# Kernel optimization log

Hardware: AMD Instinct MI355X
Metric: run time of the kernel (lower is better)

## Reference

```python
import jax, jax.numpy as jnp
import numpy as np

C = 64   # in_planes
F = 40   # n_freq
T = 512  # n_frame
B = 16


def setup_inputs() -> dict:
    key = jax.random.key(0)
    kx, kq, kk, kv = jax.random.split(key, 4)
    x = jax.random.normal(kx, (B, C, F, T), dtype=jnp.float32)
    # 1x1 conv weights, no bias: [out_ch, in_ch]
    s = 1.0 / np.sqrt(C)
    Wq = jax.random.uniform(kq, (C, C), dtype=jnp.float32, minval=-s, maxval=s)
    Wk = jax.random.uniform(kk, (C, C), dtype=jnp.float32, minval=-s, maxval=s)
    Wv = jax.random.uniform(kv, (C, C), dtype=jnp.float32, minval=-s, maxval=s)
    return {"x": x, "Wq": Wq, "Wk": Wk, "Wv": Wv}


def _proj_tokens(W, x):
    # 1x1 conv (channel mix) then permute(0,3,2,1) + view -> [B, T, F*C]
    y = jnp.einsum('oc,bcft->btfo', W, x)      # [B, T, F, C]
    b, t, f, c = y.shape
    return y.reshape(b, t, f * c)


def reference(x, Wq, Wk, Wv):
    n_batch, n_planes, n_freq, n_frame = x.shape
    d = n_freq * n_planes
    q = _proj_tokens(Wq, x)                     # [B, T, d]
    k = _proj_tokens(Wk, x)
    v = _proj_tokens(Wv, x)
    scores = jnp.einsum('bqd,bkd->bqk', q, k) / jnp.sqrt(jnp.float32(d))
    attn = jax.nn.softmax(scores, axis=-1)      # [B, T, T]
    out = jnp.einsum('bqk,bkd->bqd', attn, v)   # [B, T, d]
    out = out.reshape(n_batch, n_frame, n_freq, n_planes)
    return jnp.transpose(out, (0, 3, 2, 1))     # [B, C, F, T]
```

## Files before the change

kernel.cpp:

```cpp
#include <hip/hip_runtime.h>

constexpr int B_ = 16, C_ = 64, F_ = 40, T_ = 512;
constexpr int D_ = F_ * C_;
constexpr float SCALE = 0.019764235376052372f;

typedef __attribute__((ext_vector_type(8))) short s16x8;
typedef __attribute__((ext_vector_type(4))) short s16x4;
typedef __attribute__((ext_vector_type(2))) short s16x2;
typedef __attribute__((ext_vector_type(4))) float f32x4;

static __device__ __forceinline__ short f2bf(float f) {
  union { float f; unsigned u; } v; v.f = f;
  unsigned r = v.u + 0x7fffu + ((v.u >> 16) & 1u);
  return (short)(r >> 16);
}

static __device__ __forceinline__ f32x4 mfma16(s16x8 a, s16x8 b, f32x4 c) {
  return __builtin_amdgcn_mfma_f32_16x16x32_bf16(a, b, c, 0, 0, 0);
}

__global__ __launch_bounds__(256) void proj_kernel(
    const float* __restrict__ x,
    const float* __restrict__ Wq, const float* __restrict__ Wk,
    const float* __restrict__ Wv,
    short* __restrict__ Q, short* __restrict__ K, short* __restrict__ V)
{
  constexpr int WS = 72;
  constexpr int XS = 260;
  __shared__ short Wl[3][64 * WS];
  __shared__ short Xl[64 * XS];

  const int b = blockIdx.z, f = blockIdx.y, tt = blockIdx.x;
  const int tid = threadIdx.x;

  for (int i = tid; i < 64 * 64; i += 256) {
    const int o = i >> 6, c = i & 63;
    Wl[0][o * WS + c] = f2bf(Wq[i]);
    Wl[1][o * WS + c] = f2bf(Wk[i]);
    Wl[2][o * WS + c] = f2bf(Wv[i]);
  }
  const float* xp = x + (((size_t)b * 64) * 40 + f) * 512 + tt * 256;
  for (int i = tid; i < 64 * 64; i += 256) {
    const int c = i >> 6, j = i & 63;
    const float4 v4 = *(const float4*)(xp + (size_t)c * (F_ * T_) + j * 4);
    s16x4 s4; s4[0] = f2bf(v4.x); s4[1] = f2bf(v4.y);
    s4[2] = f2bf(v4.z); s4[3] = f2bf(v4.w);
    *(s16x4*)&Xl[c * XS + j * 4] = s4;
  }
  __syncthreads();

  const int w = tid >> 6, lane = tid & 63;
  const int quad = lane >> 4, c16 = lane & 15;
  const int tl = w * 64;

  s16x8 bfrag[4][2];
  #pragma unroll
  for (int ni = 0; ni < 4; ++ni)
    #pragma unroll
    for (int ks = 0; ks < 2; ++ks) {
      const int t = tl + ni * 16 + c16;
      const int cb = ks * 32 + quad * 8;
      s16x8 tmp;
      #pragma unroll
      for (int j = 0; j < 8; ++j) tmp[j] = Xl[(cb + j) * XS + t];
      bfrag[ni][ks] = tmp;
    }

  for (int p = 0; p < 3; ++p) {
    f32x4 acc[4][4] = {};
    #pragma unroll
    for (int ks = 0; ks < 2; ++ks) {
      s16x8 afrag[4];
      #pragma unroll
      for (int mi = 0; mi < 4; ++mi)
        afrag[mi] = *(const s16x8*)&Wl[p][(mi * 16 + c16) * WS + ks * 32 + quad * 8];
      #pragma unroll
      for (int mi = 0; mi < 4; ++mi)
        #pragma unroll
        for (int ni = 0; ni < 4; ++ni)
          acc[mi][ni] = mfma16(afrag[mi], bfrag[ni][ks], acc[mi][ni]);
    }
    if (p < 2) {
      short* outp = (p == 0) ? Q : K;
      #pragma unroll
      for (int mi = 0; mi < 4; ++mi)
        #pragma unroll
        for (int ni = 0; ni < 4; ++ni) {
          const int t = tt * 256 + tl + ni * 16 + c16;
          const int o = mi * 16 + quad * 4;
          s16x4 s4;
          #pragma unroll
          for (int r = 0; r < 4; ++r) s4[r] = f2bf(acc[mi][ni][r]);
          *(s16x4*)&outp[((size_t)(b * 512 + t)) * D_ + f * 64 + o] = s4;
        }
    } else {
      #pragma unroll
      for (int mi = 0; mi < 4; ++mi)
        #pragma unroll
        for (int ni = 0; ni < 4; ++ni) {
          const int t = tt * 256 + tl + ni * 16 + c16;
          #pragma unroll
          for (int r = 0; r < 4; ++r) {
            const int o = mi * 16 + quad * 4 + r;
            V[((size_t)(b * D_ + f * 64 + o)) * 512 + t] = f2bf(acc[mi][ni][r]);
          }
        }
    }
  }
}

__global__ __launch_bounds__(256) void scores_kernel(
    const short* __restrict__ Q, const short* __restrict__ K,
    float* __restrict__ S)
{
  __shared__ short As[128 * 32];
  __shared__ short Bs[128 * 32];
  const int b = blockIdx.y;
  const int mt = blockIdx.x >> 2, nt = blockIdx.x & 3;
  const int m0 = mt * 128, n0 = nt * 128;
  const int tid = threadIdx.x;
  const int w = tid >> 6, lane = tid & 63, quad = lane >> 4, c16 = lane & 15;
  const int wm = (w >> 1) * 64, wn = (w & 1) * 64;
  const int r0 = tid >> 2, cc8 = (tid & 3) * 8;

  const short* qb = Q + (size_t)b * 512 * D_;
  const short* kb = K + (size_t)b * 512 * D_;
  const short* qrow0 = qb + (size_t)(m0 + r0) * D_ + cc8;
  const short* qrow1 = qb + (size_t)(m0 + 64 + r0) * D_ + cc8;
  const short* krow0 = kb + (size_t)(n0 + r0) * D_ + cc8;
  const short* krow1 = kb + (size_t)(n0 + 64 + r0) * D_ + cc8;

  f32x4 acc[4][4] = {};
  s16x8 a0 = *(const s16x8*)(qrow0);
  s16x8 a1 = *(const s16x8*)(qrow1);
  s16x8 b0 = *(const s16x8*)(krow0);
  s16x8 b1 = *(const s16x8*)(krow1);

  constexpr int NK = D_ / 32;
  for (int kk = 0; kk < NK; ++kk) {
    __syncthreads();
    *(s16x8*)&As[r0 * 32 + cc8] = a0;
    *(s16x8*)&As[(64 + r0) * 32 + cc8] = a1;
    *(s16x8*)&Bs[r0 * 32 + cc8] = b0;
    *(s16x8*)&Bs[(64 + r0) * 32 + cc8] = b1;
    __syncthreads();
    if (kk + 1 < NK) {
      const int off = (kk + 1) * 32;
      a0 = *(const s16x8*)(qrow0 + off);
      a1 = *(const s16x8*)(qrow1 + off);
      b0 = *(const s16x8*)(krow0 + off);
      b1 = *(const s16x8*)(krow1 + off);
    }
    s16x8 am[4], bm[4];
    #pragma unroll
    for (int mi = 0; mi < 4; ++mi)
      am[mi] = *(const s16x8*)&As[(wm + mi * 16 + c16) * 32 + quad * 8];
    #pragma unroll
    for (int ni = 0; ni < 4; ++ni)
      bm[ni] = *(const s16x8*)&Bs[(wn + ni * 16 + c16) * 32 + quad * 8];
    #pragma unroll
    for (int mi = 0; mi < 4; ++mi)
      #pragma unroll
      for (int ni = 0; ni < 4; ++ni)
        acc[mi][ni] = mfma16(am[mi], bm[ni], acc[mi][ni]);
  }

  float* sp = S + (size_t)b * 512 * 512;
  #pragma unroll
  for (int mi = 0; mi < 4; ++mi)
    #pragma unroll
    for (int ni = 0; ni < 4; ++ni) {
      const int kcol = n0 + wn + ni * 16 + c16;
      const int qrow = m0 + wm + mi * 16 + quad * 4;
      #pragma unroll
      for (int r = 0; r < 4; ++r)
        sp[(size_t)(qrow + r) * 512 + kcol] = acc[mi][ni][r] * SCALE;
    }
}

__global__ __launch_bounds__(256) void softmax_kernel(
    const float* __restrict__ S, short* __restrict__ A)
{
  const int b = blockIdx.y, q = blockIdx.x;
  const int tid = threadIdx.x, w = tid >> 6, lane = tid & 63;
  const float* row = S + ((size_t)b * 512 + q) * 512;
  float2 v = *(const float2*)(row + tid * 2);

  float m = fmaxf(v.x, v.y);
  #pragma unroll
  for (int off = 1; off < 64; off <<= 1) m = fmaxf(m, __shfl_xor(m, off));
  __shared__ float redm[4], reds[4];
  if (lane == 0) redm[w] = m;
  __syncthreads();
  m = fmaxf(fmaxf(redm[0], redm[1]), fmaxf(redm[2], redm[3]));

  const float e0 = __expf(v.x - m), e1 = __expf(v.y - m);
  float s = e0 + e1;
  #pragma unroll
  for (int off = 1; off < 64; off <<= 1) s += __shfl_xor(s, off);
  if (lane == 0) reds[w] = s;
  __syncthreads();
  s = (reds[0] + reds[1]) + (reds[2] + reds[3]);

  const float inv = 1.0f / s;
  s16x2 o2; o2[0] = f2bf(e0 * inv); o2[1] = f2bf(e1 * inv);
  *(s16x2*)&A[((size_t)b * 512 + q) * 512 + tid * 2] = o2;
}

__global__ __launch_bounds__(256) void pv_kernel(
    const short* __restrict__ A, const short* __restrict__ V,
    float* __restrict__ out)
{
  __shared__ short As[128 * 32];
  __shared__ short Bs[128 * 32];
  const int b = blockIdx.y;
  const int mt = blockIdx.x / 20, dt = blockIdx.x % 20;
  const int m0 = mt * 128, n0 = dt * 128;
  const int tid = threadIdx.x;
  const int w = tid >> 6, lane = tid & 63, quad = lane >> 4, c16 = lane & 15;
  const int wm = (w >> 1) * 64, wn = (w & 1) * 64;
  const int r0 = tid >> 2, cc8 = (tid & 3) * 8;

  const short* ab = A + (size_t)b * 512 * 512;
  const short* vb = V + (size_t)b * D_ * 512;
  const short* arow0 = ab + (size_t)(m0 + r0) * 512 + cc8;
  const short* arow1 = ab + (size_t)(m0 + 64 + r0) * 512 + cc8;
  const short* vrow0 = vb + (size_t)(n0 + r0) * 512 + cc8;
  const short* vrow1 = vb + (size_t)(n0 + 64 + r0) * 512 + cc8;

  f32x4 acc[4][4] = {};
  s16x8 a0 = *(const s16x8*)(arow0);
  s16x8 a1 = *(const s16x8*)(arow1);
  s16x8 b0 = *(const s16x8*)(vrow0);
  s16x8 b1 = *(const s16x8*)(vrow1);

  constexpr int NK = 512 / 32;
  for (int kk = 0; kk < NK; ++kk) {
    __syncthreads();
    *(s16x8*)&As[r0 * 32 + cc8] = a0;
    *(s16x8*)&As[(64 + r0) * 32 + cc8] = a1;
    *(s16x8*)&Bs[r0 * 32 + cc8] = b0;
    *(s16x8*)&Bs[(64 + r0) * 32 + cc8] = b1;
    __syncthreads();
    if (kk + 1 < NK) {
      const int off = (kk + 1) * 32;
      a0 = *(const s16x8*)(arow0 + off);
      a1 = *(const s16x8*)(arow1 + off);
      b0 = *(const s16x8*)(vrow0 + off);
      b1 = *(const s16x8*)(vrow1 + off);
    }
    s16x8 am[4], bm[4];
    #pragma unroll
    for (int mi = 0; mi < 4; ++mi)
      am[mi] = *(const s16x8*)&As[(wm + mi * 16 + c16) * 32 + quad * 8];
    #pragma unroll
    for (int ni = 0; ni < 4; ++ni)
      bm[ni] = *(const s16x8*)&Bs[(wn + ni * 16 + c16) * 32 + quad * 8];
    #pragma unroll
    for (int mi = 0; mi < 4; ++mi)
      #pragma unroll
      for (int ni = 0; ni < 4; ++ni)
        acc[mi][ni] = mfma16(am[mi], bm[ni], acc[mi][ni]);
  }

  #pragma unroll
  for (int mi = 0; mi < 4; ++mi)
    #pragma unroll
    for (int ni = 0; ni < 4; ++ni) {
      const int d = n0 + wn + ni * 16 + c16;
      const int ff = d >> 6, cc = d & 63;
      const int t = m0 + wm + mi * 16 + quad * 4;
      float4 o4;
      o4.x = acc[mi][ni][0]; o4.y = acc[mi][ni][1];
      o4.z = acc[mi][ni][2]; o4.w = acc[mi][ni][3];
      *(float4*)&out[(((size_t)b * 64 + cc) * 40 + ff) * 512 + t] = o4;
    }
}

extern "C" void kernel_launch(void* const* d_in, const int* in_sizes, int n_in,
                              void* d_out, int out_size, void* d_ws, size_t ws_size,
                              hipStream_t stream)
{
  const float* x  = (const float*)d_in[0];
  const float* Wq = (const float*)d_in[1];
  const float* Wk = (const float*)d_in[2];
  const float* Wv = (const float*)d_in[3];
  float* out = (float*)d_out;

  char* ws = (char*)d_ws;
  constexpr size_t QB = (size_t)B_ * T_ * D_ * 2;
  short* Q  = (short*)(ws);
  short* Kt = (short*)(ws + QB);
  short* Vt = (short*)(ws + 2 * QB);
  float* S  = (float*)(ws + 3 * QB);
  short* At = (short*)(ws + 3 * QB + (size_t)B_ * T_ * T_ * 4);

  proj_kernel<<<dim3(2, 40, 16), 256, 0, stream>>>(x, Wq, Wk, Wv, Q, Kt, Vt);
  scores_kernel<<<dim3(16, 16), 256, 0, stream>>>(Q, Kt, S);
  softmax_kernel<<<dim3(512, 16), 256, 0, stream>>>(S, At);
  pv_kernel<<<dim3(80, 16), 256, 0, stream>>>(At, Vt, out);
}
```

Baseline: 305.0 us.

## Rebalance proj/scores grids, vectorize V stores, use per-wave softmax rows

The projection kernel now handles 128 frames per block instead of 256, doubling the grid. It drops the shared-memory weight staging and loads weights into registers straight from global memory. The V projection swaps the MFMA operand order so V can be stored as 4-wide vectors instead of scalar strided stores. The scores kernel halves its M tile to 64, doubling its grid of 256 blocks for better CU occupancy. Softmax now assigns one row per wave with shuffle-only reductions and no block barriers, at the cost of redundant weight conversion per block.

Result: slower. 320.0 us (+4.9%).

```diff
diff --git a/kernel.cpp b/kernel.cpp
--- a/kernel.cpp
+++ b/kernel.cpp
@@ -6,7 +6,6 @@
 
 typedef __attribute__((ext_vector_type(8))) short s16x8;
 typedef __attribute__((ext_vector_type(4))) short s16x4;
-typedef __attribute__((ext_vector_type(2))) short s16x2;
 typedef __attribute__((ext_vector_type(4))) float f32x4;
 
 static __device__ __forceinline__ short f2bf(float f) {
@@ -25,23 +24,17 @@
     const float* __restrict__ Wv,
     short* __restrict__ Q, short* __restrict__ K, short* __restrict__ V)
 {
-  constexpr int WS = 72;
-  constexpr int XS = 260;
-  __shared__ short Wl[3][64 * WS];
+  constexpr int XS = 132;
   __shared__ short Xl[64 * XS];
 
   const int b = blockIdx.z, f = blockIdx.y, tt = blockIdx.x;
   const int tid = threadIdx.x;
 
-  for (int i = tid; i < 64 * 64; i += 256) {
-    const int o = i >> 6, c = i & 63;
-    Wl[0][o * WS + c] = f2bf(Wq[i]);
-    Wl[1][o * WS + c] = f2bf(Wk[i]);
-    Wl[2][o * WS + c] = f2bf(Wv[i]);
-  }
-  const float* xp = x + (((size_t)b * 64) * 40 + f) * 512 + tt * 256;
-  for (int i = tid; i < 64 * 64; i += 256) {
-    const int c = i >> 6, j = i & 63;
+  const float* xp = x + (((size_t)b * 64) * 40 + f) * 512 + tt * 128;
+  #pragma unroll
+  for (int it = 0; it < 8; ++it) {
+    const int i = tid + it * 256;
+    const int c = i >> 5, j = i & 31;
     const float4 v4 = *(const float4*)(xp + (size_t)c * (F_ * T_) + j * 4);
     s16x4 s4; s4[0] = f2bf(v4.x); s4[1] = f2bf(v4.y);
     s4[2] = f2bf(v4.z); s4[3] = f2bf(v4.w);
@@ -51,11 +44,11 @@
 
   const int w = tid >> 6, lane = tid & 63;
   const int quad = lane >> 4, c16 = lane & 15;
-  const int tl = w * 64;
-
-  s16x8 bfrag[4][2];
-  #pragma unroll
-  for (int ni = 0; ni < 4; ++ni)
+  const int tl = w * 32;
+
+  s16x8 bfrag[2][2];
+  #pragma unroll
+  for (int ni = 0; ni < 2; ++ni)
     #pragma unroll
     for (int ks = 0; ks < 2; ++ks) {
       const int t = tl + ni * 16 + c16;
@@ -66,27 +59,38 @@
       bfrag[ni][ks] = tmp;
     }
 
+  #pragma unroll
   for (int p = 0; p < 3; ++p) {
-    f32x4 acc[4][4] = {};
-    #pragma unroll
-    for (int ks = 0; ks < 2; ++ks) {
-      s16x8 afrag[4];
-      #pragma unroll
-      for (int mi = 0; mi < 4; ++mi)
-        afrag[mi] = *(const s16x8*)&Wl[p][(mi * 16 + c16) * WS + ks * 32 + quad * 8];
+    const float* Wp = (p == 0) ? Wq : (p == 1) ? Wk : Wv;
+    s16x8 wfrag[4][2];
+    #pragma unroll
+    for (int mi = 0; mi < 4; ++mi)
+      #pragma unroll
+      for (int ks = 0; ks < 2; ++ks) {
+        const float* wp = Wp + (mi * 16 + c16) * 64 + ks * 32 + quad * 8;
+        const float4 w0 = *(const float4*)(wp);
+        const float4 w1 = *(const float4*)(wp + 4);
+        s16x8 wf;
+        wf[0] = f2bf(w0.x); wf[1] = f2bf(w0.y); wf[2] = f2bf(w0.z); wf[3] = f2bf(w0.w);
+        wf[4] = f2bf(w1.x); wf[5] = f2bf(w1.y); wf[6] = f2bf(w1.z); wf[7] = f2bf(w1.w);
+        wfrag[mi][ks] = wf;
+      }
+
+    if (p < 2) {
+      f32x4 acc[4][2] = {};
+      #pragma unroll
+      for (int ks = 0; ks < 2; ++ks)
+        #pragma unroll
+        for (int mi = 0; mi < 4; ++mi)
+          #pragma unroll
+          for (int ni = 0; ni < 2; ++ni)
+            acc[mi][ni] = mfma16(wfrag[mi][ks], bfrag[ni][ks], acc[mi][ni]);
+      short* outp = (p == 0) ? Q : K;
       #pragma unroll
       for (int mi = 0; mi < 4; ++mi)
         #pragma unroll
-        for (int ni = 0; ni < 4; ++ni)
-          acc[mi][ni] = mfma16(afrag[mi], bfrag[ni][ks], acc[mi][ni]);
-    }
-    if (p < 2) {
-      short* outp = (p == 0) ? Q : K;
-      #pragma unroll
-      for (int mi = 0; mi < 4; ++mi)
-        #pragma unroll
-        for (int ni = 0; ni < 4; ++ni) {
-          const int t = tt * 256 + tl + ni * 16 + c16;
+        for (int ni = 0; ni < 2; ++ni) {
+          const int t = tt * 128 + tl + ni * 16 + c16;
           const int o = mi * 16 + quad * 4;
           s16x4 s4;
           #pragma unroll
@@ -94,16 +98,24 @@
           *(s16x4*)&outp[((size_t)(b * 512 + t)) * D_ + f * 64 + o] = s4;
         }
     } else {
-      #pragma unroll
-      for (int mi = 0; mi < 4; ++mi)
+      f32x4 acc[2][4] = {};
+      #pragma unroll
+      for (int ks = 0; ks < 2; ++ks)
         #pragma unroll
-        for (int ni = 0; ni < 4; ++ni) {
-          const int t = tt * 256 + tl + ni * 16 + c16;
+        for (int ni = 0; ni < 2; ++ni)
           #pragma unroll
-          for (int r = 0; r < 4; ++r) {
-            const int o = mi * 16 + quad * 4 + r;
-            V[((size_t)(b * D_ + f * 64 + o)) * 512 + t] = f2bf(acc[mi][ni][r]);
-          }
+          for (int mi = 0; mi < 4; ++mi)
+            acc[ni][mi] = mfma16(bfrag[ni][ks], wfrag[mi][ks], acc[ni][mi]);
+      #pragma unroll
+      for (int ni = 0; ni < 2; ++ni)
+        #pragma unroll
+        for (int mi = 0; mi < 4; ++mi) {
+          const int t = tt * 128 + tl + ni * 16 + quad * 4;
+          const int o = mi * 16 + c16;
+          s16x4 s4;
+          #pragma unroll
+          for (int r = 0; r < 4; ++r) s4[r] = f2bf(acc[ni][mi][r]);
+          *(s16x4*)&V[((size_t)(b * D_ + f * 64 + o)) * 512 + t] = s4;
         }
     }
   }
@@ -113,26 +125,22 @@
     const short* __restrict__ Q, const short* __restrict__ K,
     float* __restrict__ S)
 {
-  __shared__ short As[128 * 32];
+  __shared__ short As[64 * 32];
   __shared__ short Bs[128 * 32];
   const int b = blockIdx.y;
   const int mt = blockIdx.x >> 2, nt = blockIdx.x & 3;
-  const int m0 = mt * 128, n0 = nt * 128;
+  const int m0 = mt * 64, n0 = nt * 128;
   const int tid = threadIdx.x;
   const int w = tid >> 6, lane = tid & 63, quad = lane >> 4, c16 = lane & 15;
-  const int wm = (w >> 1) * 64, wn = (w & 1) * 64;
+  const int wm = (w >> 1) * 32, wn = (w & 1) * 64;
   const int r0 = tid >> 2, cc8 = (tid & 3) * 8;
 
-  const short* qb = Q + (size_t)b * 512 * D_;
-  const short* kb = K + (size_t)b * 512 * D_;
-  const short* qrow0 = qb + (size_t)(m0 + r0) * D_ + cc8;
-  const short* qrow1 = qb + (size_t)(m0 + 64 + r0) * D_ + cc8;
-  const short* krow0 = kb + (size_t)(n0 + r0) * D_ + cc8;
-  const short* krow1 = kb + (size_t)(n0 + 64 + r0) * D_ + cc8;
-
-  f32x4 acc[4][4] = {};
-  s16x8 a0 = *(const s16x8*)(qrow0);
-  s16x8 a1 = *(const s16x8*)(qrow1);
+  const short* qrow  = Q + ((size_t)(b * 512 + m0 + r0)) * D_ + cc8;
+  const short* krow0 = K + ((size_t)(b * 512 + n0 + r0)) * D_ + cc8;
+  const short* krow1 = krow0 + (size_t)64 * D_;
+
+  f32x4 acc[2][4] = {};
+  s16x8 a0 = *(const s16x8*)(qrow);
   s16x8 b0 = *(const s16x8*)(krow0);
   s16x8 b1 = *(const s16x8*)(krow1);
 
@@ -140,26 +148,24 @@
   for (int kk = 0; kk < NK; ++kk) {
     __syncthreads();
     *(s16x8*)&As[r0 * 32 + cc8] = a0;
-    *(s16x8*)&As[(64 + r0) * 32 + cc8] = a1;
     *(s16x8*)&Bs[r0 * 32 + cc8] = b0;
     *(s16x8*)&Bs[(64 + r0) * 32 + cc8] = b1;
     __syncthreads();
     if (kk + 1 < NK) {
       const int off = (kk + 1) * 32;
-      a0 = *(const s16x8*)(qrow0 + off);
-      a1 = *(const s16x8*)(qrow1 + off);
+      a0 = *(const s16x8*)(qrow + off);
       b0 = *(const s16x8*)(krow0 + off);
       b1 = *(const s16x8*)(krow1 + off);
     }
-    s16x8 am[4], bm[4];
-    #pragma unroll
-    for (int mi = 0; mi < 4; ++mi)
+    s16x8 am[2], bm[4];
+    #pragma unroll
+    for (int mi = 0; mi < 2; ++mi)
       am[mi] = *(const s16x8*)&As[(wm + mi * 16 + c16) * 32 + quad * 8];
     #pragma unroll
     for (int ni = 0; ni < 4; ++ni)
       bm[ni] = *(const s16x8*)&Bs[(wn + ni * 16 + c16) * 32 + quad * 8];
     #pragma unroll
-    for (int mi = 0; mi < 4; ++mi)
+    for (int mi = 0; mi < 2; ++mi)
       #pragma unroll
       for (int ni = 0; ni < 4; ++ni)
         acc[mi][ni] = mfma16(am[mi], bm[ni], acc[mi][ni]);
@@ -167,44 +173,48 @@
 
   float* sp = S + (size_t)b * 512 * 512;
   #pragma unroll
-  for (int mi = 0; mi < 4; ++mi)
+  for (int mi = 0; mi < 2; ++mi)
     #pragma unroll
     for (int ni = 0; ni < 4; ++ni) {
       const int kcol = n0 + wn + ni * 16 + c16;
-      const int qrow = m0 + wm + mi * 16 + quad * 4;
+      const int qrow_o = m0 + wm + mi * 16 + quad * 4;
       #pragma unroll
       for (int r = 0; r < 4; ++r)
-        sp[(size_t)(qrow + r) * 512 + kcol] = acc[mi][ni][r] * SCALE;
+        sp[(size_t)(qrow_o + r) * 512 + kcol] = acc[mi][ni][r] * SCALE;
     }
 }
 
 __global__ __launch_bounds__(256) void softmax_kernel(
     const float* __restrict__ S, short* __restrict__ A)
 {
-  const int b = blockIdx.y, q = blockIdx.x;
+  const int b = blockIdx.y;
   const int tid = threadIdx.x, w = tid >> 6, lane = tid & 63;
+  const int q = blockIdx.x * 4 + w;
   const float* row = S + ((size_t)b * 512 + q) * 512;
-  float2 v = *(const float2*)(row + tid * 2);
-
-  float m = fmaxf(v.x, v.y);
+
+  const float4 v0 = *(const float4*)(row + lane * 4);
+  const float4 v1 = *(const float4*)(row + 256 + lane * 4);
+  float e[8] = {v0.x, v0.y, v0.z, v0.w, v1.x, v1.y, v1.z, v1.w};
+
+  float m = e[0];
+  #pragma unroll
+  for (int i = 1; i < 8; ++i) m = fmaxf(m, e[i]);
   #pragma unroll
   for (int off = 1; off < 64; off <<= 1) m = fmaxf(m, __shfl_xor(m, off));
-  __shared__ float redm[4], reds[4];
-  if (lane == 0) redm[w] = m;
-  __syncthreads();
-  m = fmaxf(fmaxf(redm[0], redm[1]), fmaxf(redm[2], redm[3]));
-
-  const float e0 = __expf(v.x - m), e1 = __expf(v.y - m);
-  float s = e0 + e1;
+
+  float s = 0.f;
+  #pragma unroll
+  for (int i = 0; i < 8; ++i) { e[i] = __expf(e[i] - m); s += e[i]; }
   #pragma unroll
   for (int off = 1; off < 64; off <<= 1) s += __shfl_xor(s, off);
-  if (lane == 0) reds[w] = s;
-  __syncthreads();
-  s = (reds[0] + reds[1]) + (reds[2] + reds[3]);
 
   const float inv = 1.0f / s;
-  s16x2 o2; o2[0] = f2bf(e0 * inv); o2[1] = f2bf(e1 * inv);
-  *(s16x2*)&A[((size_t)b * 512 + q) * 512 + tid * 2] = o2;
+  short* arow = A + ((size_t)b * 512 + q) * 512;
+  s16x4 o0, o1;
+  #pragma unroll
+  for (int i = 0; i < 4; ++i) { o0[i] = f2bf(e[i] * inv); o1[i] = f2bf(e[i + 4] * inv); }
+  *(s16x4*)&arow[lane * 4] = o0;
+  *(s16x4*)&arow[256 + lane * 4] = o1;
 }
 
 __global__ __launch_bounds__(256) void pv_kernel(
@@ -295,8 +305,8 @@
   float* S  = (float*)(ws + 3 * QB);
   short* At = (short*)(ws + 3 * QB + (size_t)B_ * T_ * T_ * 4);
 
-  proj_kernel<<<dim3(2, 40, 16), 256, 0, stream>>>(x, Wq, Wk, Wv, Q, Kt, Vt);
-  scores_kernel<<<dim3(16, 16), 256, 0, stream>>>(Q, Kt, S);
-  softmax_kernel<<<dim3(512, 16), 256, 0, stream>>>(S, At);
+  proj_kernel<<<dim3(4, 40, 16), 256, 0, stream>>>(x, Wq, Wk, Wv, Q, Kt, Vt);
+  scores_kernel<<<dim3(32, 16), 256, 0, stream>>>(Q, Kt, S);
+  softmax_kernel<<<dim3(128, 16), 256, 0, stream>>>(S, At);
   pv_kernel<<<dim3(80, 16), 256, 0, stream>>>(At, Vt, out);
 }
```
